# Kernel tuning notes

Measured on AMD Instinct MI355X. Metric: run time of the kernel, lower is better.

The kernel has to match this reference:

```python
import jax, jax.numpy as jnp
import numpy as np

B, DIM, H, W = 1, 64, 128, 128
WS = 7  # window_size


def setup_inputs() -> dict:
    key = jax.random.key(0)
    ks = jax.random.split(key, 7)
    scale = 1.0 / np.sqrt(DIM).astype(np.float32)
    x = jax.random.normal(ks[0], (B, DIM, H, W), jnp.float32)
    Wq = jax.random.normal(ks[1], (DIM, DIM), jnp.float32) * scale
    bq = jax.random.normal(ks[2], (DIM,), jnp.float32) * 0.01
    Wk = jax.random.normal(ks[3], (DIM, DIM), jnp.float32) * scale
    bk = jax.random.normal(ks[4], (DIM,), jnp.float32) * 0.01
    Wv = jax.random.normal(ks[5], (DIM, DIM), jnp.float32) * scale
    bv = jax.random.normal(ks[6], (DIM,), jnp.float32) * 0.01
    return {"x": x, "Wq": Wq, "bq": bq, "Wk": Wk, "bk": bk, "Wv": Wv, "bv": bv}


def _conv1x1(x, Wt, b):
    # nn.Conv2d(dim, dim, kernel_size=1): out[b,o,h,w] = sum_c W[o,c]*x[b,c,h,w] + b[o]
    return jnp.einsum('bchw,oc->bohw', x, Wt) + b[None, :, None, None]


def _windows(t, ws):
    # zero-pad then extract ws x ws sliding windows -> (B, C, H, W, ws*ws)
    b, c, h, w = t.shape
    pad = ws // 2
    tp = jnp.pad(t, ((0, 0), (0, 0), (pad, pad), (pad, pad)))
    return jnp.stack([tp[:, :, i:i + h, j:j + w]
                      for i in range(ws) for j in range(ws)], axis=-1)


def reference(x, Wq, bq, Wk, bk, Wv, bv):
    q = _conv1x1(x, Wq, bq)
    k = _conv1x1(x, Wk, bk)
    v = _conv1x1(x, Wv, bv)
    qw = _windows(q, WS)  # (B,C,H,W,P)
    kw = _windows(k, WS)
    vw = _windows(v, WS)
    # row-wise attention: position (h,w) attends to (h,k) over width,
    # contracting channels and window taps p (exact math of the torch einsum)
    attn = jnp.einsum('bchwp,bchkp->bhwk', qw, kw)
    attn = jax.nn.softmax(attn, axis=-1)
    # fuse the weighted sum and the final sum over p into one einsum
    out = jnp.einsum('bhwk,bchkp->bchw', attn, vw)
    return out
```

## Files before the change

### kernel.cpp

```cpp
#include <hip/hip_runtime.h>

static constexpr int C    = 64;
static constexpr int H    = 128;
static constexpr int W    = 128;
static constexpr int NPIX = H * W;
static constexpr int PAD  = 3;

__global__ __launch_bounds__(256, 4) void k_conv(
    const float* __restrict__ x,
    const float* __restrict__ Wq, const float* __restrict__ bq,
    const float* __restrict__ Wk, const float* __restrict__ bk,
    const float* __restrict__ Wv, const float* __restrict__ bv,
    float* __restrict__ qT, float* __restrict__ ko, float* __restrict__ vo)
{
    const int tid  = threadIdx.x;
    const int lane = tid & 63;
    const int p    = blockIdx.x * 64 + lane;
    const int o0   = __builtin_amdgcn_readfirstlane(
                         blockIdx.y * 32 + (tid >> 6) * 8);
    const int z    = blockIdx.z;
    const float* Wm = (z == 0) ? Wq : (z == 1) ? Wk : Wv;
    const float* bm = (z == 0) ? bq : (z == 1) ? bk : bv;

    float xr[C];
#pragma unroll
    for (int c = 0; c < C; ++c) xr[c] = x[c * NPIX + p];

    float acc[8];
#pragma unroll
    for (int j = 0; j < 8; ++j) acc[j] = bm[o0 + j];

#pragma unroll
    for (int c = 0; c < C; ++c) {
        const float xv = xr[c];
#pragma unroll
        for (int j = 0; j < 8; ++j)
            acc[j] += Wm[(o0 + j) * C + c] * xv;
    }

    if (z == 0) {
        *(float4*)(qT + (size_t)p * C + o0) =
            make_float4(acc[0], acc[1], acc[2], acc[3]);
        *(float4*)(qT + (size_t)p * C + o0 + 4) =
            make_float4(acc[4], acc[5], acc[6], acc[7]);
    } else {
        float* outm = (z == 1) ? ko : vo;
#pragma unroll
        for (int j = 0; j < 8; ++j)
            outm[(o0 + j) * NPIX + p] = acc[j];
    }
}

__global__ __launch_bounds__(256, 4) void k_mid(
    const float* __restrict__ qT, const float* __restrict__ kmat,
    const float* __restrict__ v,
    float* __restrict__ Sd, float* __restrict__ Vs)
{
    __shared__ union {
        struct { float Sl[22][130]; float qs[22][64]; } g;
        struct { float vt[22][128]; float vh[22][128]; } box;
    } u;
    const int bid = blockIdx.x;
    const int tid = threadIdx.x;

    if (bid < 1024) {
        const int h   = bid >> 3;
        const int w0  = (bid & 7) * 16;
        const int kk  = tid & 127;
        const int wsl = tid >> 7;

        for (int i = tid; i < 22 * 16; i += 256) {
            int r  = i >> 4, c4 = (i & 15) << 2;
            int wp = w0 - 3 + r;
            float4 qv = make_float4(0.f, 0.f, 0.f, 0.f);
            if (wp >= 0 && wp < W)
                qv = *(const float4*)(qT + (size_t)(h * W + wp) * C + c4);
            *(float4*)(&u.g.qs[r][c4]) = qv;
        }

        float ksr[C];
#pragma unroll
        for (int c = 0; c < C; ++c) ksr[c] = kmat[c * NPIX + h * W + kk];
        __syncthreads();

        for (int j = 0; j < 11; ++j) {
            int row = wsl * 11 + j;
            float a0 = 0.f, a1 = 0.f, a2 = 0.f, a3 = 0.f;
#pragma unroll
            for (int c = 0; c < C; c += 4) {
                float4 qv = *(const float4*)(&u.g.qs[row][c]);
                a0 += qv.x * ksr[c + 0];
                a1 += qv.y * ksr[c + 1];
                a2 += qv.z * ksr[c + 2];
                a3 += qv.w * ksr[c + 3];
            }
            u.g.Sl[row][kk] = (a0 + a1) + (a2 + a3);
        }
        __syncthreads();

#pragma unroll
        for (int r = 0; r < 8; ++r) {
            int wl = wsl * 8 + r;
            float a = 0.f;
#pragma unroll
            for (int dd = -PAD; dd <= PAD; ++dd) {
                int kj = kk + dd;
                if (kj >= 0 && kj < W)
                    a += u.g.Sl[wl + 3 + dd][kj];
            }
            Sd[(size_t)(h * W + w0 + wl) * W + kk] = a;
        }
    } else {
        const int b2 = bid - 1024;
        const int c  = b2 >> 3;
        const int h0 = (b2 & 7) * 16;

        for (int i = tid; i < 22 * 128; i += 256) {
            int r = i >> 7, w = i & 127;
            int h = h0 - 3 + r;
            u.box.vt[r][w] = (h >= 0 && h < H) ? v[c * NPIX + h * W + w] : 0.f;
        }
        __syncthreads();
        for (int i = tid; i < 22 * 128; i += 256) {
            int r = i >> 7, w = i & 127;
            float s = 0.f;
#pragma unroll
            for (int d = -PAD; d <= PAD; ++d) {
                int wj = w + d;
                if (wj >= 0 && wj < W) s += u.box.vt[r][wj];
            }
            u.box.vh[r][w] = s;
        }
        __syncthreads();
        for (int i = tid; i < 16 * 128; i += 256) {
            int r = i >> 7, w = i & 127;
            float s = 0.f;
#pragma unroll
            for (int d = 0; d < 7; ++d) s += u.box.vh[r + d][w];
            Vs[c * NPIX + (h0 + r) * W + w] = s;
        }
    }
}

__global__ __launch_bounds__(512, 2) void k_fused(
    const float* __restrict__ Sd, const float* __restrict__ Vs,
    float* __restrict__ out)
{
    constexpr int AP = 129;
    __shared__ float At[64][AP];
    __shared__ float Vl[64][128];

    const int h   = blockIdx.x;
    const int w0  = blockIdx.y * 64;
    const int tid = threadIdx.x;

    float4 vstage[4];
#pragma unroll
    for (int r = 0; r < 4; ++r) {
        int L  = tid + r * 512;
        int c  = L >> 5;
        int k4 = (L & 31) << 2;
        vstage[r] = *(const float4*)(Vs + (size_t)c * NPIX + h * W + k4);
    }

    const int wl = tid >> 3;
    const int s  = tid & 7;

    float4 g0 = make_float4(0.f, 0.f, 0.f, 0.f);
    float4 g1 = g0, g2 = g0, g3 = g0;
#pragma unroll
    for (int i = 0; i < 7; ++i) {
        int hp = h - 3 + i;
        if (hp >= 0 && hp < H) {
            const float4* src = (const float4*)(
                Sd + (size_t)hp * NPIX + (w0 + wl) * W + s * 16);
            float4 a = src[0], b = src[1], c2 = src[2], d = src[3];
            g0.x += a.x;  g0.y += a.y;  g0.z += a.z;  g0.w += a.w;
            g1.x += b.x;  g1.y += b.y;  g1.z += b.z;  g1.w += b.w;
            g2.x += c2.x; g2.y += c2.y; g2.z += c2.z; g2.w += c2.w;
            g3.x += d.x;  g3.y += d.y;  g3.z += d.z;  g3.w += d.w;
        }
    }

    float lg[16] = { g0.x, g0.y, g0.z, g0.w,  g1.x, g1.y, g1.z, g1.w,
                     g2.x, g2.y, g2.z, g2.w,  g3.x, g3.y, g3.z, g3.w };

    float m = lg[0];
#pragma unroll
    for (int e = 1; e < 16; ++e) m = fmaxf(m, lg[e]);
#pragma unroll
    for (int off = 1; off <= 4; off <<= 1) m = fmaxf(m, __shfl_xor(m, off));

    float ssum = 0.f;
#pragma unroll
    for (int e = 0; e < 16; ++e) { lg[e] = __expf(lg[e] - m); ssum += lg[e]; }
#pragma unroll
    for (int off = 1; off <= 4; off <<= 1) ssum += __shfl_xor(ssum, off);
    const float inv = 1.f / ssum;

#pragma unroll
    for (int e = 0; e < 16; ++e) At[wl][s * 16 + e] = lg[e] * inv;

#pragma unroll
    for (int r = 0; r < 4; ++r) {
        int L  = tid + r * 512;
        int c  = L >> 5;
        int k4 = (L & 31) << 2;
        *(float4*)(&Vl[c][k4]) = vstage[r];
    }
    __syncthreads();

    const int w2 = tid & 63;
    const int c0 = __builtin_amdgcn_readfirstlane((tid >> 6) * 8);

    float acc[8];
#pragma unroll
    for (int j = 0; j < 8; ++j) acc[j] = 0.f;

    for (int kk = 0; kk < 128; kk += 4) {
        float4 a = *(const float4*)(&At[w2][kk]);
#pragma unroll
        for (int j = 0; j < 8; ++j) {
            float4 vv = *(const float4*)(&Vl[c0 + j][kk]);
            acc[j] += a.x * vv.x + a.y * vv.y + a.z * vv.z + a.w * vv.w;
        }
    }

#pragma unroll
    for (int j = 0; j < 8; ++j)
        out[(size_t)(c0 + j) * NPIX + h * W + w0 + w2] = acc[j];
}

extern "C" void kernel_launch(void* const* d_in, const int* in_sizes, int n_in,
                              void* d_out, int out_size, void* d_ws, size_t ws_size,
                              hipStream_t stream)
{
    const float* x  = (const float*)d_in[0];
    const float* Wq = (const float*)d_in[1];
    const float* bq = (const float*)d_in[2];
    const float* Wk = (const float*)d_in[3];
    const float* bk = (const float*)d_in[4];
    const float* Wv = (const float*)d_in[5];
    const float* bv = (const float*)d_in[6];
    float* out = (float*)d_out;

    float* ws = (float*)d_ws;
    const size_t NQ = (size_t)C * NPIX;
    const size_t NS = (size_t)H * W * W;

    float* qT   = ws;
    float* k    = ws + NQ;
    float* v    = ws + 2 * NQ;
    float* Sd   = ws + 3 * NQ;
    float* Vsum = ws + 3 * NQ + NS;

    k_conv<<<dim3(NPIX / 64, 2, 3), 256, 0, stream>>>(x, Wq, bq, Wk, bk, Wv, bv, qT, k, v);
    k_mid<<<dim3(1536), 256, 0, stream>>>(qT, k, v, Sd, Vsum);
    k_fused<<<dim3(H, 2), 512, 0, stream>>>(Sd, Vsum, out);
}
```

Before: 124.7 us.

## Fuse 1x1 conv projections into row-score kernel and move vertical V box-sum into output kernel

Merges the three-way 1x1 conv and the Q·K row-score and horizontal V box-filter stages into one per-row kernel that keeps q, k, v in LDS, removing the q/k/v round trip through global memory and one launch. The vertical 7-tap sum of V is moved into the final softmax/weighted-sum kernel, which now reads seven rows of horizontally summed V. The cost is redundant conv work: each (h, half-row) block recomputes the projections for the whole 128-wide row. It also uses large LDS (about 130 KB) and only 256 blocks of 512 threads, which limits occupancy.

```diff
diff --git a/kernel.cpp b/kernel.cpp
--- a/kernel.cpp
+++ b/kernel.cpp
@@ -4,146 +4,130 @@
 static constexpr int H    = 128;
 static constexpr int W    = 128;
 static constexpr int NPIX = H * W;
-static constexpr int PAD  = 3;
-
-__global__ __launch_bounds__(256, 4) void k_conv(
+
+__global__ __launch_bounds__(512, 2) void k_rowA(
     const float* __restrict__ x,
     const float* __restrict__ Wq, const float* __restrict__ bq,
     const float* __restrict__ Wk, const float* __restrict__ bk,
     const float* __restrict__ Wv, const float* __restrict__ bv,
-    float* __restrict__ qT, float* __restrict__ ko, float* __restrict__ vo)
+    float* __restrict__ Sd, float* __restrict__ vh)
 {
-    const int tid  = threadIdx.x;
+    __shared__ float lds[33280];
+    float (*xs)[128]  = (float(*)[128])(lds);
+    float (*vs)[128]  = (float(*)[128])(lds + 8192);
+    float (*qs2)[136] = (float(*)[136])(lds + 16384);
+    float (*ks)[128]  = (float(*)[128])(lds + 25088);
+    float (*G)[132]   = (float(*)[132])(lds);
+
+    const int h   = blockIdx.x;
+    const int w0  = blockIdx.y * 64;
+    const int tid = threadIdx.x;
+
+#pragma unroll
+    for (int r = 0; r < 4; ++r) {
+        int f  = tid + r * 512;
+        int c  = f >> 5;
+        int k4 = (f & 31) << 2;
+        *(float4*)(&xs[c][k4]) =
+            *(const float4*)(x + (size_t)c * NPIX + h * W + k4);
+    }
+    {
+        int c   = tid >> 3;
+        int g   = tid & 7;
+        int col = (g < 3) ? g : (g + 128);
+        qs2[c][col] = 0.f;
+    }
+    __syncthreads();
+
+    {
+        const int col = tid & 127;
+        const int c0  = __builtin_amdgcn_readfirstlane((tid >> 7) * 16);
+
+        float aq[16], ak[16], av[16];
+#pragma unroll
+        for (int j = 0; j < 16; ++j) {
+            aq[j] = bq[c0 + j]; ak[j] = bk[c0 + j]; av[j] = bv[c0 + j];
+        }
+#pragma unroll 4
+        for (int c = 0; c < 64; ++c) {
+            const float xv = xs[c][col];
+#pragma unroll
+            for (int j = 0; j < 16; ++j) {
+                aq[j] += Wq[(c0 + j) * 64 + c] * xv;
+                ak[j] += Wk[(c0 + j) * 64 + c] * xv;
+                av[j] += Wv[(c0 + j) * 64 + c] * xv;
+            }
+        }
+#pragma unroll
+        for (int j = 0; j < 16; ++j) {
+            qs2[c0 + j][col + 3] = aq[j];
+            ks [c0 + j][col]     = ak[j];
+            vs [c0 + j][col]     = av[j];
+        }
+    }
+    __syncthreads();
+
     const int lane = tid & 63;
-    const int p    = blockIdx.x * 64 + lane;
-    const int o0   = __builtin_amdgcn_readfirstlane(
-                         blockIdx.y * 32 + (tid >> 6) * 8);
-    const int z    = blockIdx.z;
-    const float* Wm = (z == 0) ? Wq : (z == 1) ? Wk : Wv;
-    const float* bm = (z == 0) ? bq : (z == 1) ? bk : bv;
-
-    float xr[C];
-#pragma unroll
-    for (int c = 0; c < C; ++c) xr[c] = x[c * NPIX + p];
-
-    float acc[8];
-#pragma unroll
-    for (int j = 0; j < 8; ++j) acc[j] = bm[o0 + j];
-
-#pragma unroll
-    for (int c = 0; c < C; ++c) {
-        const float xv = xr[c];
-#pragma unroll
-        for (int j = 0; j < 8; ++j)
-            acc[j] += Wm[(o0 + j) * C + c] * xv;
-    }
-
-    if (z == 0) {
-        *(float4*)(qT + (size_t)p * C + o0) =
-            make_float4(acc[0], acc[1], acc[2], acc[3]);
-        *(float4*)(qT + (size_t)p * C + o0 + 4) =
-            make_float4(acc[4], acc[5], acc[6], acc[7]);
-    } else {
-        float* outm = (z == 1) ? ko : vo;
-#pragma unroll
-        for (int j = 0; j < 8; ++j)
-            outm[(o0 + j) * NPIX + p] = acc[j];
+    const int wg8  = tid >> 6;
+
+#pragma unroll
+    for (int j = 0; j < 8; ++j) {
+        int c = wg8 * 8 + j;
+        float s = 0.f;
+#pragma unroll
+        for (int d = -3; d <= 3; ++d) {
+            int wj = w0 + lane + d;
+            if (wj >= 0 && wj < W) s += vs[c][wj];
+        }
+        vh[(size_t)c * NPIX + h * W + w0 + lane] = s;
+    }
+
+    float k0[64], k1[64];
+#pragma unroll
+    for (int c = 0; c < 64; ++c) {
+        k0[c] = ks[c][lane];
+        k1[c] = ks[c][lane + 64];
+    }
+    __syncthreads();
+
+    for (int tile = wg8; tile < 18; tile += 8) {
+        float ax0 = 0.f, ax1 = 0.f, ay0 = 0.f, ay1 = 0.f;
+        float az0 = 0.f, az1 = 0.f, aw0 = 0.f, aw1 = 0.f;
+#pragma unroll
+        for (int c = 0; c < 64; ++c) {
+            float4 qv = *(const float4*)(&qs2[c][w0 + 4 * tile]);
+            ax0 += qv.x * k0[c]; ax1 += qv.x * k1[c];
+            ay0 += qv.y * k0[c]; ay1 += qv.y * k1[c];
+            az0 += qv.z * k0[c]; az1 += qv.z * k1[c];
+            aw0 += qv.w * k0[c]; aw1 += qv.w * k1[c];
+        }
+        const int wl4 = 4 * tile;
+        G[wl4 + 0][lane] = ax0;  G[wl4 + 0][lane + 64] = ax1;
+        G[wl4 + 1][lane] = ay0;  G[wl4 + 1][lane + 64] = ay1;
+        G[wl4 + 2][lane] = az0;  G[wl4 + 2][lane + 64] = az1;
+        G[wl4 + 3][lane] = aw0;  G[wl4 + 3][lane + 64] = aw1;
+    }
+    __syncthreads();
+
+    {
+        const int kk  = tid & 127;
+        const int wg4 = tid >> 7;
+#pragma unroll
+        for (int r = 0; r < 16; ++r) {
+            int wl = wg4 * 16 + r;
+            float s = 0.f;
+#pragma unroll
+            for (int j = 0; j < 7; ++j) {
+                int kj = kk + j - 3;
+                if (kj >= 0 && kj < W) s += G[wl + j][kj];
+            }
+            Sd[((size_t)h * W + w0 + wl) * W + kk] = s;
+        }
     }
 }
 
-__global__ __launch_bounds__(256, 4) void k_mid(
-    const float* __restrict__ qT, const float* __restrict__ kmat,
-    const float* __restrict__ v,
-    float* __restrict__ Sd, float* __restrict__ Vs)
-{
-    __shared__ union {
-        struct { float Sl[22][130]; float qs[22][64]; } g;
-        struct { float vt[22][128]; float vh[22][128]; } box;
-    } u;
-    const int bid = blockIdx.x;
-    const int tid = threadIdx.x;
-
-    if (bid < 1024) {
-        const int h   = bid >> 3;
-        const int w0  = (bid & 7) * 16;
-        const int kk  = tid & 127;
-        const int wsl = tid >> 7;
-
-        for (int i = tid; i < 22 * 16; i += 256) {
-            int r  = i >> 4, c4 = (i & 15) << 2;
-            int wp = w0 - 3 + r;
-            float4 qv = make_float4(0.f, 0.f, 0.f, 0.f);
-            if (wp >= 0 && wp < W)
-                qv = *(const float4*)(qT + (size_t)(h * W + wp) * C + c4);
-            *(float4*)(&u.g.qs[r][c4]) = qv;
-        }
-
-        float ksr[C];
-#pragma unroll
-        for (int c = 0; c < C; ++c) ksr[c] = kmat[c * NPIX + h * W + kk];
-        __syncthreads();
-
-        for (int j = 0; j < 11; ++j) {
-            int row = wsl * 11 + j;
-            float a0 = 0.f, a1 = 0.f, a2 = 0.f, a3 = 0.f;
-#pragma unroll
-            for (int c = 0; c < C; c += 4) {
-                float4 qv = *(const float4*)(&u.g.qs[row][c]);
-                a0 += qv.x * ksr[c + 0];
-                a1 += qv.y * ksr[c + 1];
-                a2 += qv.z * ksr[c + 2];
-                a3 += qv.w * ksr[c + 3];
-            }
-            u.g.Sl[row][kk] = (a0 + a1) + (a2 + a3);
-        }
-        __syncthreads();
-
-#pragma unroll
-        for (int r = 0; r < 8; ++r) {
-            int wl = wsl * 8 + r;
-            float a = 0.f;
-#pragma unroll
-            for (int dd = -PAD; dd <= PAD; ++dd) {
-                int kj = kk + dd;
-                if (kj >= 0 && kj < W)
-                    a += u.g.Sl[wl + 3 + dd][kj];
-            }
-            Sd[(size_t)(h * W + w0 + wl) * W + kk] = a;
-        }
-    } else {
-        const int b2 = bid - 1024;
-        const int c  = b2 >> 3;
-        const int h0 = (b2 & 7) * 16;
-
-        for (int i = tid; i < 22 * 128; i += 256) {
-            int r = i >> 7, w = i & 127;
-            int h = h0 - 3 + r;
-            u.box.vt[r][w] = (h >= 0 && h < H) ? v[c * NPIX + h * W + w] : 0.f;
-        }
-        __syncthreads();
-        for (int i = tid; i < 22 * 128; i += 256) {
-            int r = i >> 7, w = i & 127;
-            float s = 0.f;
-#pragma unroll
-            for (int d = -PAD; d <= PAD; ++d) {
-                int wj = w + d;
-                if (wj >= 0 && wj < W) s += u.box.vt[r][wj];
-            }
-            u.box.vh[r][w] = s;
-        }
-        __syncthreads();
-        for (int i = tid; i < 16 * 128; i += 256) {
-            int r = i >> 7, w = i & 127;
-            float s = 0.f;
-#pragma unroll
-            for (int d = 0; d < 7; ++d) s += u.box.vh[r + d][w];
-            Vs[c * NPIX + (h0 + r) * W + w] = s;
-        }
-    }
-}
-
-__global__ __launch_bounds__(512, 2) void k_fused(
-    const float* __restrict__ Sd, const float* __restrict__ Vs,
+__global__ __launch_bounds__(512, 2) void k_rowB(
+    const float* __restrict__ Sd, const float* __restrict__ vh,
     float* __restrict__ out)
 {
     constexpr int AP = 129;
@@ -154,13 +138,22 @@
     const int w0  = blockIdx.y * 64;
     const int tid = threadIdx.x;
 
-    float4 vstage[4];
-#pragma unroll
-    for (int r = 0; r < 4; ++r) {
-        int L  = tid + r * 512;
-        int c  = L >> 5;
-        int k4 = (L & 31) << 2;
-        vstage[r] = *(const float4*)(Vs + (size_t)c * NPIX + h * W + k4);
+    float4 va[4];
+#pragma unroll
+    for (int r = 0; r < 4; ++r) va[r] = make_float4(0.f, 0.f, 0.f, 0.f);
+#pragma unroll
+    for (int i = 0; i < 7; ++i) {
+        int hp = h - 3 + i;
+        if (hp >= 0 && hp < H) {
+#pragma unroll
+            for (int r = 0; r < 4; ++r) {
+                int L  = tid + r * 512;
+                int c  = L >> 5;
+                int k4 = (L & 31) << 2;
+                float4 t = *(const float4*)(vh + (size_t)c * NPIX + hp * W + k4);
+                va[r].x += t.x; va[r].y += t.y; va[r].z += t.z; va[r].w += t.w;
+            }
+        }
     }
 
     const int wl = tid >> 3;
@@ -206,7 +199,7 @@
         int L  = tid + r * 512;
         int c  = L >> 5;
         int k4 = (L & 31) << 2;
-        *(float4*)(&Vl[c][k4]) = vstage[r];
+        *(float4*)(&Vl[c][k4]) = va[r];
     }
     __syncthreads();
 
@@ -245,16 +238,11 @@
     float* out = (float*)d_out;
 
     float* ws = (float*)d_ws;
-    const size_t NQ = (size_t)C * NPIX;
     const size_t NS = (size_t)H * W * W;
 
-    float* qT   = ws;
-    float* k    = ws + NQ;
-    float* v    = ws + 2 * NQ;
-    float* Sd   = ws + 3 * NQ;
-    float* Vsum = ws + 3 * NQ + NS;
-
-    k_conv<<<dim3(NPIX / 64, 2, 3), 256, 0, stream>>>(x, Wq, bq, Wk, bk, Wv, bv, qT, k, v);
-    k_mid<<<dim3(1536), 256, 0, stream>>>(qT, k, v, Sd, Vsum);
-    k_fused<<<dim3(H, 2), 512, 0, stream>>>(Sd, Vsum, out);
+    float* Sd = ws;
+    float* vh = ws + NS;
+
+    k_rowA<<<dim3(H, 2), 512, 0, stream>>>(x, Wq, bq, Wk, bk, Wv, bv, Sd, vh);
+    k_rowB<<<dim3(H, 2), 512, 0, stream>>>(Sd, vh, out);
 }
```

Result: slower. 144.0 us (+15.5%).

## Stage conv weights in LDS and widen attention-apply blocks to 1024 threads

Applied to the files above, without the earlier changes.

The 1x1 conv kernel now loads each 64x64 weight matrix into shared memory once per block. Each block computes all 64 output channels for its pixels, so x is read once per projection instead of twice, and each thread produces 16 outputs. The fused softmax/apply kernel moves to 1024-thread blocks with half the per-thread work, which raises parallelism per row. The trade-offs are more LDS traffic and register pressure in the conv, and a launch bound of 1024 threads with min 4 blocks that may not be achievable given the kernel's ~66KB of LDS.

```diff
diff --git a/kernel.cpp b/kernel.cpp
--- a/kernel.cpp
+++ b/kernel.cpp
@@ -13,40 +13,53 @@
     const float* __restrict__ Wv, const float* __restrict__ bv,
     float* __restrict__ qT, float* __restrict__ ko, float* __restrict__ vo)
 {
+    __shared__ float Wl[64][64];
     const int tid  = threadIdx.x;
     const int lane = tid & 63;
     const int p    = blockIdx.x * 64 + lane;
-    const int o0   = __builtin_amdgcn_readfirstlane(
-                         blockIdx.y * 32 + (tid >> 6) * 8);
-    const int z    = blockIdx.z;
+    const int o0   = __builtin_amdgcn_readfirstlane((tid >> 6) * 16);
+    const int z    = blockIdx.y;
     const float* Wm = (z == 0) ? Wq : (z == 1) ? Wk : Wv;
     const float* bm = (z == 0) ? bq : (z == 1) ? bk : bv;
 
-    float xr[C];
-#pragma unroll
-    for (int c = 0; c < C; ++c) xr[c] = x[c * NPIX + p];
-
-    float acc[8];
-#pragma unroll
-    for (int j = 0; j < 8; ++j) acc[j] = bm[o0 + j];
-
-#pragma unroll
-    for (int c = 0; c < C; ++c) {
-        const float xv = xr[c];
-#pragma unroll
-        for (int j = 0; j < 8; ++j)
-            acc[j] += Wm[(o0 + j) * C + c] * xv;
+#pragma unroll
+    for (int r = 0; r < 4; ++r) {
+        int f = tid + r * 256;
+        int o = f >> 4, c4 = (f & 15) << 2;
+        *(float4*)(&Wl[o][c4]) = *(const float4*)(Wm + o * 64 + c4);
+    }
+    __syncthreads();
+
+    float acc[16];
+#pragma unroll
+    for (int j = 0; j < 16; ++j) acc[j] = bm[o0 + j];
+
+#pragma unroll
+    for (int half = 0; half < 2; ++half) {
+        float xr[32];
+#pragma unroll
+        for (int c = 0; c < 32; ++c)
+            xr[c] = x[(half * 32 + c) * NPIX + p];
+#pragma unroll
+        for (int c4 = 0; c4 < 32; c4 += 4) {
+#pragma unroll
+            for (int j = 0; j < 16; ++j) {
+                float4 wv = *(const float4*)(&Wl[o0 + j][half * 32 + c4]);
+                acc[j] += wv.x * xr[c4 + 0] + wv.y * xr[c4 + 1]
+                        + wv.z * xr[c4 + 2] + wv.w * xr[c4 + 3];
+            }
+        }
     }
 
     if (z == 0) {
-        *(float4*)(qT + (size_t)p * C + o0) =
-            make_float4(acc[0], acc[1], acc[2], acc[3]);
-        *(float4*)(qT + (size_t)p * C + o0 + 4) =
-            make_float4(acc[4], acc[5], acc[6], acc[7]);
+#pragma unroll
+        for (int j = 0; j < 16; j += 4)
+            *(float4*)(qT + (size_t)p * C + o0 + j) =
+                make_float4(acc[j], acc[j + 1], acc[j + 2], acc[j + 3]);
     } else {
         float* outm = (z == 1) ? ko : vo;
 #pragma unroll
-        for (int j = 0; j < 8; ++j)
+        for (int j = 0; j < 16; ++j)
             outm[(o0 + j) * NPIX + p] = acc[j];
     }
 }
@@ -142,7 +155,7 @@
     }
 }
 
-__global__ __launch_bounds__(512, 2) void k_fused(
+__global__ __launch_bounds__(1024, 4) void k_fused(
     const float* __restrict__ Sd, const float* __restrict__ Vs,
     float* __restrict__ out)
 {
@@ -154,56 +167,53 @@
     const int w0  = blockIdx.y * 64;
     const int tid = threadIdx.x;
 
-    float4 vstage[4];
-#pragma unroll
-    for (int r = 0; r < 4; ++r) {
-        int L  = tid + r * 512;
+    float4 vstage[2];
+#pragma unroll
+    for (int r = 0; r < 2; ++r) {
+        int L  = tid + r * 1024;
         int c  = L >> 5;
         int k4 = (L & 31) << 2;
         vstage[r] = *(const float4*)(Vs + (size_t)c * NPIX + h * W + k4);
     }
 
-    const int wl = tid >> 3;
-    const int s  = tid & 7;
+    const int wl = tid >> 4;
+    const int s  = tid & 15;
 
     float4 g0 = make_float4(0.f, 0.f, 0.f, 0.f);
-    float4 g1 = g0, g2 = g0, g3 = g0;
+    float4 g1 = g0;
 #pragma unroll
     for (int i = 0; i < 7; ++i) {
         int hp = h - 3 + i;
         if (hp >= 0 && hp < H) {
             const float4* src = (const float4*)(
-                Sd + (size_t)hp * NPIX + (w0 + wl) * W + s * 16);
-            float4 a = src[0], b = src[1], c2 = src[2], d = src[3];
-            g0.x += a.x;  g0.y += a.y;  g0.z += a.z;  g0.w += a.w;
-            g1.x += b.x;  g1.y += b.y;  g1.z += b.z;  g1.w += b.w;
-            g2.x += c2.x; g2.y += c2.y; g2.z += c2.z; g2.w += c2.w;
-            g3.x += d.x;  g3.y += d.y;  g3.z += d.z;  g3.w += d.w;
-        }
-    }
-
-    float lg[16] = { g0.x, g0.y, g0.z, g0.w,  g1.x, g1.y, g1.z, g1.w,
-                     g2.x, g2.y, g2.z, g2.w,  g3.x, g3.y, g3.z, g3.w };
+                Sd + (size_t)hp * NPIX + (w0 + wl) * W + s * 8);
+            float4 a = src[0], b = src[1];
+            g0.x += a.x; g0.y += a.y; g0.z += a.z; g0.w += a.w;
+            g1.x += b.x; g1.y += b.y; g1.z += b.z; g1.w += b.w;
+        }
+    }
+
+    float lg[8] = { g0.x, g0.y, g0.z, g0.w,  g1.x, g1.y, g1.z, g1.w };
 
     float m = lg[0];
 #pragma unroll
-    for (int e = 1; e < 16; ++e) m = fmaxf(m, lg[e]);
-#pragma unroll
-    for (int off = 1; off <= 4; off <<= 1) m = fmaxf(m, __shfl_xor(m, off));
+    for (int e = 1; e < 8; ++e) m = fmaxf(m, lg[e]);
+#pragma unroll
+    for (int off = 1; off <= 8; off <<= 1) m = fmaxf(m, __shfl_xor(m, off));
 
     float ssum = 0.f;
 #pragma unroll
-    for (int e = 0; e < 16; ++e) { lg[e] = __expf(lg[e] - m); ssum += lg[e]; }
-#pragma unroll
-    for (int off = 1; off <= 4; off <<= 1) ssum += __shfl_xor(ssum, off);
+    for (int e = 0; e < 8; ++e) { lg[e] = __expf(lg[e] - m); ssum += lg[e]; }
+#pragma unroll
+    for (int off = 1; off <= 8; off <<= 1) ssum += __shfl_xor(ssum, off);
     const float inv = 1.f / ssum;
 
 #pragma unroll
-    for (int e = 0; e < 16; ++e) At[wl][s * 16 + e] = lg[e] * inv;
-
-#pragma unroll
-    for (int r = 0; r < 4; ++r) {
-        int L  = tid + r * 512;
+    for (int e = 0; e < 8; ++e) At[wl][s * 8 + e] = lg[e] * inv;
+
+#pragma unroll
+    for (int r = 0; r < 2; ++r) {
+        int L  = tid + r * 1024;
         int c  = L >> 5;
         int k4 = (L & 31) << 2;
         *(float4*)(&Vl[c][k4]) = vstage[r];
@@ -211,23 +221,23 @@
     __syncthreads();
 
     const int w2 = tid & 63;
-    const int c0 = __builtin_amdgcn_readfirstlane((tid >> 6) * 8);
-
-    float acc[8];
-#pragma unroll
-    for (int j = 0; j < 8; ++j) acc[j] = 0.f;
+    const int c0 = __builtin_amdgcn_readfirstlane((tid >> 6) * 4);
+
+    float acc[4];
+#pragma unroll
+    for (int j = 0; j < 4; ++j) acc[j] = 0.f;
 
     for (int kk = 0; kk < 128; kk += 4) {
         float4 a = *(const float4*)(&At[w2][kk]);
 #pragma unroll
-        for (int j = 0; j < 8; ++j) {
+        for (int j = 0; j < 4; ++j) {
             float4 vv = *(const float4*)(&Vl[c0 + j][kk]);
             acc[j] += a.x * vv.x + a.y * vv.y + a.z * vv.z + a.w * vv.w;
         }
     }
 
 #pragma unroll
-    for (int j = 0; j < 8; ++j)
+    for (int j = 0; j < 4; ++j)
         out[(size_t)(c0 + j) * NPIX + h * W + w0 + w2] = acc[j];
 }
 
@@ -254,7 +264,7 @@
     float* Sd   = ws + 3 * NQ;
     float* Vsum = ws + 3 * NQ + NS;
 
-    k_conv<<<dim3(NPIX / 64, 2, 3), 256, 0, stream>>>(x, Wq, bq, Wk, bk, Wv, bv, qT, k, v);
+    k_conv<<<dim3(NPIX / 64, 3), 256, 0, stream>>>(x, Wq, bq, Wk, bk, Wv, bv, qT, k, v);
     k_mid<<<dim3(1536), 256, 0, stream>>>(qT, k, v, Sd, Vsum);
-    k_fused<<<dim3(H, 2), 512, 0, stream>>>(Sd, Vsum, out);
-}
+    k_fused<<<dim3(H, 2), 1024, 0, stream>>>(Sd, Vsum, out);
+}
```

New measurement: 154.6 us. 1.24x slower.
